# Kernel tuning notes

Hardware: AMD Instinct MI355X
Metric: run time of the kernel (lower is better)

Reference implementation:

```python
import jax, jax.numpy as jnp
import numpy as np

EPS_THRESH = 1e-10   # threshold used by GraphFilter to sparsify A
NORM_EPS = 1e-12     # torch F.normalize clamp
REG = 2.0 / 3.0      # AGE preprocess_graph reg coefficient (layer=1)


def setup_inputs() -> dict:
    key = jax.random.key(0)
    X = jax.random.normal(key, (8192, 512), dtype=jnp.float32)
    return {"X": X}


def reference(X):
    N = X.shape[0]
    # row L2-normalize (torch F.normalize semantics)
    norms = jnp.maximum(jnp.linalg.norm(X, axis=1, keepdims=True), NORM_EPS)
    feats = X / norms
    # dense cosine-similarity graph, thresholded at epsilon
    A = feats @ feats.T                               # [N, N]
    A = jnp.where(A < EPS_THRESH, 0.0, A)
    # remove self-loops (adj - diag_sparse in the original)
    idx = jnp.arange(N)
    A = A.at[idx, idx].set(0.0)
    # preprocess_graph(norm='sym', renorm=True): adj_ = A + I, sym-normalize
    rowsum = jnp.sum(A, axis=1) + 1.0                 # diag of (A + I)
    d_inv_sqrt = rowsum ** -0.5
    A_norm = A * d_inv_sqrt[:, None] * d_inv_sqrt[None, :]
    # A+I normalized: off-diag from A_norm, diag contributes d_i^-1
    diag_term = d_inv_sqrt * d_inv_sqrt               # = 1/rowsum
    # filter = I - reg * (I - (A_norm + diag(diag_term)))
    #        = (1-reg) I + reg * (A_norm + diag(diag_term))
    # propagate: out = filter @ X
    out = (1.0 - REG) * X + REG * (A_norm @ X + (diag_term[:, None] * X))
    return out
```

## Files before the change

kernel.cpp:

```cpp
#include <hip/hip_runtime.h>


#define NR 8192
#define DC 512
#define KZN 4

typedef unsigned short u16;
typedef signed char i8;
typedef float f32x4 __attribute__((ext_vector_type(4)));
typedef int i32x4 __attribute__((ext_vector_type(4)));
typedef u16 u16x4 __attribute__((ext_vector_type(4)));

#define QF_INV 453.5714285f
#define DEQA   4.8608093e-6f
#define QS_INV 254.0f
#define QY_INV 211.6666666f
#define DEQ    1.8600229e-5f

__device__ __forceinline__ float bf2f(u16 u) {
  union { unsigned u; float f; } v; v.u = ((unsigned)u) << 16; return v.f;
}
__device__ __forceinline__ u16 f2bf(float f) {
  union { float f; unsigned u; } v; v.f = f;
  unsigned r = v.u + 0x7fffu + ((v.u >> 16) & 1u);
  return (u16)(r >> 16);
}

__device__ __forceinline__ void async16(const void* ga, void* la) {
  __builtin_amdgcn_global_load_lds(
      (const __attribute__((address_space(1))) unsigned int*)ga,
      (__attribute__((address_space(3))) unsigned int*)la, 16, 0, 0);
}

template <int ROWS, int NT>
__device__ __forceinline__ void stage_i8_k128(const i8* __restrict__ g, int ld,
                                              int row0, int k0, i8* lds, int tid) {
  constexpr int PER = (ROWS * 8) / NT;
#pragma unroll
  for (int q = 0; q < PER; ++q) {
    int s = q * NT + tid;
    int r = s >> 3;
    int kq = (s & 7) ^ (r & 7);
    async16(g + (size_t)(row0 + r) * ld + (k0 + kq * 16), lds + s * 16);
  }
}
__device__ __forceinline__ i32x4 frag_i8_k128(const i8* lds, int m, int c) {
  int phys = c ^ (m & 7);
  return *(const i32x4*)(lds + m * 128 + phys * 16);
}

__global__ __launch_bounds__(256) void k_normalize(const float* __restrict__ X,
                                                   i8* __restrict__ F,
                                                   float* __restrict__ rs_partial) {
  int row = blockIdx.x;
  int tid = threadIdx.x;
  if (tid == 0) rs_partial[row] = 0.f;
  const float* xr = X + (size_t)row * DC;
  float2 v = *(const float2*)(xr + 2 * tid);
  float s = v.x * v.x + v.y * v.y;
#pragma unroll
  for (int off = 32; off; off >>= 1) s += __shfl_down(s, off);
  __shared__ float wsum[4];
  if ((tid & 63) == 0) wsum[tid >> 6] = s;
  __syncthreads();
  float tot = wsum[0] + wsum[1] + wsum[2] + wsum[3];
  float scale = QF_INV / fmaxf(sqrtf(tot), 1e-12f);
  int q0 = (int)rintf(v.x * scale);
  int q1 = (int)rintf(v.y * scale);
  q0 = q0 > 127 ? 127 : (q0 < -127 ? -127 : q0);
  q1 = q1 > 127 ? 127 : (q1 < -127 ? -127 : q1);
  u16 pk = (u16)((q0 & 255) | ((q1 & 255) << 8));
  ((u16*)(F + (size_t)row * DC))[tid] = pk;
}

__global__ __launch_bounds__(256, 4) void k_simgemm(const i8* __restrict__ F,
                                                    i8* __restrict__ S,
                                                    float* __restrict__ rs_partial) {
  __shared__ alignas(16) char smem[32768];
  i8* As = (i8*)smem;
  i8* Bs = (i8*)(smem + 16384);
  int tid = threadIdx.x, lane = tid & 63, wave = tid >> 6;
  int b = blockIdx.x;
  int tj = (int)((sqrtf(8.f * b + 1.f) - 1.f) * 0.5f);
  while ((tj + 1) * (tj + 2) / 2 <= b) ++tj;
  while (tj * (tj + 1) / 2 > b) --tj;
  int ti = b - tj * (tj + 1) / 2;
  bool diag = (ti == tj);

  int wm = wave >> 1, wn = wave & 1;
  int quad = lane >> 4, col = lane & 15;
  i32x4 zero = {0, 0, 0, 0};
  i32x4 acc[4][4];
#pragma unroll
  for (int a = 0; a < 4; ++a)
#pragma unroll
    for (int c = 0; c < 4; ++c) acc[a][c] = zero;

  const i8* Bsrc = diag ? As : Bs;
  for (int kt = 0; kt < DC; kt += 128) {
    __syncthreads();
    stage_i8_k128<128, 256>(F, DC, ti * 128, kt, As, tid);
    if (!diag) stage_i8_k128<128, 256>(F, DC, tj * 128, kt, Bs, tid);
    __syncthreads();
#pragma unroll
    for (int kc = 0; kc < 2; ++kc) {
      i32x4 af[4], bfr[4];
#pragma unroll
      for (int mi = 0; mi < 4; ++mi)
        af[mi] = frag_i8_k128(As, wm * 64 + mi * 16 + col, kc * 4 + quad);
#pragma unroll
      for (int ni = 0; ni < 4; ++ni)
        bfr[ni] = frag_i8_k128(Bsrc, wn * 64 + ni * 16 + col, kc * 4 + quad);
#pragma unroll
      for (int mi = 0; mi < 4; ++mi)
#pragma unroll
        for (int ni = 0; ni < 4; ++ni)
          acc[mi][ni] = __builtin_amdgcn_mfma_i32_16x16x64_i8(af[mi], bfr[ni], acc[mi][ni], 0, 0, 0);
    }
  }

  float av[4][4][4];
  float cs[4] = {0.f, 0.f, 0.f, 0.f};
  float rv[16];
#pragma unroll
  for (int u = 0; u < 16; ++u) rv[u] = 0.f;
#pragma unroll
  for (int mi = 0; mi < 4; ++mi) {
#pragma unroll
    for (int r = 0; r < 4; ++r) {
      int gi = ti * 128 + wm * 64 + mi * 16 + quad * 4 + r;
#pragma unroll
      for (int ni = 0; ni < 4; ++ni) {
        int gj = tj * 128 + wn * 64 + ni * 16 + col;
        float v = (float)acc[mi][ni][r] * DEQA;
        if (v < 1e-10f || gi == gj) v = 0.f;
        av[mi][ni][r] = v;
        cs[ni] += v;
        rv[mi * 4 + r] += v;
      }
    }
  }
#pragma unroll
  for (int ni = 0; ni < 4; ++ni) {
    float c = cs[ni];
    c += __shfl_xor(c, 16);
    c += __shfl_xor(c, 32);
    if (quad == 0) {
      int gj = tj * 128 + wn * 64 + ni * 16 + col;
      atomicAdd(&rs_partial[gj], c);
    }
  }
  if (!diag) {
#pragma unroll
    for (int u = 0; u < 16; ++u) {
      float c = rv[u];
      c += __shfl_xor(c, 1);
      c += __shfl_xor(c, 2);
      c += __shfl_xor(c, 4);
      c += __shfl_xor(c, 8);
      if (col == 0) {
        int mi = u >> 2, r = u & 3;
        int gi = ti * 128 + wm * 64 + mi * 16 + quad * 4 + r;
        atomicAdd(&rs_partial[gi], c);
      }
    }
  }

  char* direct = smem;
  char* mirror = smem + 16384;
  __syncthreads();
#pragma unroll
  for (int mi = 0; mi < 4; ++mi) {
#pragma unroll
    for (int ni = 0; ni < 4; ++ni) {
      int cg = wn * 64 + ni * 16 + col;
      int q[4];
#pragma unroll
      for (int r = 0; r < 4; ++r) {
        int qq = (int)rintf(av[mi][ni][r] * QS_INV);
        q[r] = qq > 127 ? 127 : qq;
      }
#pragma unroll
      for (int r = 0; r < 4; ++r) {
        int row = wm * 64 + mi * 16 + quad * 4 + r;
        int chunk = (cg >> 4) ^ (row & 7);
        direct[row * 128 + chunk * 16 + (cg & 15)] = (char)q[r];
      }
      if (!diag) {
        int mcb = wm * 64 + mi * 16 + quad * 4;
        int chunk = (mcb >> 4) ^ (cg & 7);
        unsigned pk = (unsigned)(q[0] & 255) | ((unsigned)(q[1] & 255) << 8) |
                      ((unsigned)(q[2] & 255) << 16) | ((unsigned)(q[3] & 255) << 24);
        *(unsigned*)(mirror + cg * 128 + chunk * 16 + (mcb & 15)) = pk;
      }
    }
  }
  __syncthreads();
  {
    int r2 = tid >> 1, half = tid & 1;
#pragma unroll
    for (int k = 0; k < 4; ++k) {
      int c = half * 4 + k;
      int phys = c ^ (r2 & 7);
      i32x4 d = *(const i32x4*)(direct + r2 * 128 + phys * 16);
      *(i32x4*)(S + (size_t)(ti * 128 + r2) * NR + tj * 128 + c * 16) = d;
    }
    if (!diag) {
#pragma unroll
      for (int k = 0; k < 4; ++k) {
        int c = half * 4 + k;
        int phys = c ^ (r2 & 7);
        i32x4 d = *(const i32x4*)(mirror + r2 * 128 + phys * 16);
        *(i32x4*)(S + (size_t)(tj * 128 + r2) * NR + ti * 128 + c * 16) = d;
      }
    }
  }
}

__global__ __launch_bounds__(256) void k_make_yt(const float* __restrict__ X,
                                                 const float* __restrict__ rs_partial,
                                                 i8* __restrict__ Yt) {
  __shared__ float T[64][65];
  int i0 = blockIdx.x * 64, k0 = blockIdx.y * 64;
  int tid = threadIdx.x;
  {
    int iL = tid >> 2, ks = (tid & 3) * 4;
    const float* xr = X + (size_t)(i0 + iL) * DC + k0;
#pragma unroll
    for (int u = 0; u < 4; ++u) {
      float4 f = *(const float4*)(xr + ks + u * 16);
      T[iL][ks + u * 16 + 0] = f.x;
      T[iL][ks + u * 16 + 1] = f.y;
      T[iL][ks + u * 16 + 2] = f.z;
      T[iL][ks + u * 16 + 3] = f.w;
    }
  }
  __syncthreads();
  {
    int kL = tid >> 2, ib = (tid & 3) * 16;
    char pk[16];
#pragma unroll
    for (int u = 0; u < 16; ++u) {
      float dj = rsqrtf(rs_partial[i0 + ib + u] + 1.0f);
      float v = T[ib + u][kL] * dj;
      int q = (int)rintf(v * QY_INV);
      q = q > 127 ? 127 : (q < -127 ? -127 : q);
      pk[u] = (char)q;
    }
    *(i32x4*)(Yt + (size_t)(k0 + kL) * NR + i0 + ib) = *(const i32x4*)pk;
  }
}

__global__ __launch_bounds__(512, 4) void k_outgemm(const i8* __restrict__ S,
                                                    const i8* __restrict__ Yt,
                                                    u16* __restrict__ Pb) {
  __shared__ alignas(16) i8 As[128 * 128];
  __shared__ alignas(16) i8 Bs[256 * 128];
  int tid = threadIdx.x, lane = tid & 63, wave = tid >> 6;
  int tn = blockIdx.x, ti = blockIdx.y, kz = blockIdx.z;
  int wm = wave & 1, wn = wave >> 1;
  int quad = lane >> 4, col = lane & 15;
  i32x4 zero = {0, 0, 0, 0};
  i32x4 acc[4][4];
#pragma unroll
  for (int a = 0; a < 4; ++a)
#pragma unroll
    for (int c = 0; c < 4; ++c) acc[a][c] = zero;

  const int KCH = NR / KZN;
  int k_lo = kz * KCH, k_hi = k_lo + KCH;
  for (int kt = k_lo; kt < k_hi; kt += 128) {
    __syncthreads();
    stage_i8_k128<128, 512>(S, NR, ti * 128, kt, As, tid);
    stage_i8_k128<256, 512>(Yt, NR, tn * 256, kt, Bs, tid);
    __syncthreads();
#pragma unroll
    for (int kc = 0; kc < 2; ++kc) {
      i32x4 af[4], bfr[4];
#pragma unroll
      for (int mi = 0; mi < 4; ++mi)
        af[mi] = frag_i8_k128(As, wm * 64 + mi * 16 + col, kc * 4 + quad);
#pragma unroll
      for (int ni = 0; ni < 4; ++ni)
        bfr[ni] = frag_i8_k128(Bs, wn * 64 + ni * 16 + col, kc * 4 + quad);
#pragma unroll
      for (int mi = 0; mi < 4; ++mi)
#pragma unroll
        for (int ni = 0; ni < 4; ++ni)
          acc[mi][ni] = __builtin_amdgcn_mfma_i32_16x16x64_i8(af[mi], bfr[ni], acc[mi][ni], 0, 0, 0);
    }
  }
#pragma unroll
  for (int mi = 0; mi < 4; ++mi) {
#pragma unroll
    for (int r = 0; r < 4; ++r) {
      int gi = ti * 128 + wm * 64 + mi * 16 + quad * 4 + r;
#pragma unroll
      for (int ni = 0; ni < 4; ++ni) {
        int gj = tn * 256 + wn * 64 + ni * 16 + col;
        Pb[((size_t)kz * NR + gi) * DC + gj] = f2bf((float)acc[mi][ni][r] * DEQ);
      }
    }
  }
}

__global__ __launch_bounds__(256) void k_reduce(const u16* __restrict__ Pb,
                                               const float* __restrict__ X,
                                               const float* __restrict__ rs_partial,
                                               float* __restrict__ out) {
  const float c1 = (float)(2.0 / 3.0);
  const float c0 = 1.0f - c1;
  size_t idx = ((size_t)blockIdx.x * 256 + threadIdx.x) * 4;
  int i = (int)(idx >> 9);
  float4 s = {0.f, 0.f, 0.f, 0.f};
#pragma unroll
  for (int kz = 0; kz < KZN; ++kz) {
    u16x4 p = *(const u16x4*)(Pb + (size_t)kz * NR * DC + idx);
    s.x += bf2f(p[0]); s.y += bf2f(p[1]); s.z += bf2f(p[2]); s.w += bf2f(p[3]);
  }
  float4 x = *(const float4*)(X + idx);
  float rs = rs_partial[i] + 1.0f;
  float sc = c1 * rsqrtf(rs);
  float xs = c0 + c1 / rs;
  float4 o = {xs * x.x + sc * s.x, xs * x.y + sc * s.y,
              xs * x.z + sc * s.z, xs * x.w + sc * s.w};
  *(float4*)(out + idx) = o;
}

extern "C" void kernel_launch(void* const* d_in, const int* in_sizes, int n_in,
                              void* d_out, int out_size, void* d_ws, size_t ws_size,
                              hipStream_t stream) {
  const float* X = (const float*)d_in[0];
  float* out = (float*)d_out;
  char* ws = (char*)d_ws;
  i8*  S  = (i8*)(ws);
  i8*  F  = (i8*)(ws + 67108864);
  i8*  Yt = (i8*)(ws + 71303168);
  float* rs_partial = (float*)(ws + 75497472);
  u16* Pb = (u16*)(ws + 75530240);

  k_normalize<<<dim3(NR), dim3(256), 0, stream>>>(X, F, rs_partial);
  k_simgemm<<<dim3(64 * 65 / 2), dim3(256), 0, stream>>>(F, S, rs_partial);
  k_make_yt<<<dim3(128, 8), dim3(256), 0, stream>>>(X, rs_partial, Yt);
  k_outgemm<<<dim3(2, 64, KZN), dim3(512), 0, stream>>>(S, Yt, Pb);
  k_reduce<<<dim3(NR * DC / 1024), dim3(256), 0, stream>>>(Pb, X, rs_partial, out);
}
```

Measured before the change: 182.0 us.

## Load int8 MFMA fragments directly from global with register double-buffering

```diff
diff --git a/kernel.cpp b/kernel.cpp
--- a/kernel.cpp
+++ b/kernel.cpp
@@ -73,12 +73,10 @@
   ((u16*)(F + (size_t)row * DC))[tid] = pk;
 }
 
-__global__ __launch_bounds__(256, 4) void k_simgemm(const i8* __restrict__ F,
+__global__ __launch_bounds__(256, 3) void k_simgemm(const i8* __restrict__ F,
                                                     i8* __restrict__ S,
                                                     float* __restrict__ rs_partial) {
   __shared__ alignas(16) char smem[32768];
-  i8* As = (i8*)smem;
-  i8* Bs = (i8*)(smem + 16384);
   int tid = threadIdx.x, lane = tid & 63, wave = tid >> 6;
   int b = blockIdx.x;
   int tj = (int)((sqrtf(8.f * b + 1.f) - 1.f) * 0.5f);
@@ -96,26 +94,57 @@
 #pragma unroll
     for (int c = 0; c < 4; ++c) acc[a][c] = zero;
 
-  const i8* Bsrc = diag ? As : Bs;
+  const i8* pa = F + ((ti * 128 + wm * 64 + col) * DC + quad * 16);
+  const i8* pb = F + ((tj * 128 + wn * 64 + col) * DC + quad * 16);
+  bool reuse = diag && (wm == wn);
+
+  i32x4 a0[4], b0[4], a1[4], b1[4];
+#pragma unroll
+  for (int mi = 0; mi < 4; ++mi) a0[mi] = *(const i32x4*)(pa + mi * 16 * DC + 0);
+  if (!reuse) {
+#pragma unroll
+    for (int ni = 0; ni < 4; ++ni) b0[ni] = *(const i32x4*)(pb + ni * 16 * DC + 0);
+  }
+#pragma unroll
+  for (int mi = 0; mi < 4; ++mi) a1[mi] = *(const i32x4*)(pa + mi * 16 * DC + 64);
+  if (!reuse) {
+#pragma unroll
+    for (int ni = 0; ni < 4; ++ni) b1[ni] = *(const i32x4*)(pb + ni * 16 * DC + 64);
+  }
+
+#pragma unroll
   for (int kt = 0; kt < DC; kt += 128) {
-    __syncthreads();
-    stage_i8_k128<128, 256>(F, DC, ti * 128, kt, As, tid);
-    if (!diag) stage_i8_k128<128, 256>(F, DC, tj * 128, kt, Bs, tid);
-    __syncthreads();
-#pragma unroll
-    for (int kc = 0; kc < 2; ++kc) {
-      i32x4 af[4], bfr[4];
+    {
+      i32x4* B = reuse ? a0 : b0;
 #pragma unroll
       for (int mi = 0; mi < 4; ++mi)
-        af[mi] = frag_i8_k128(As, wm * 64 + mi * 16 + col, kc * 4 + quad);
-#pragma unroll
-      for (int ni = 0; ni < 4; ++ni)
-        bfr[ni] = frag_i8_k128(Bsrc, wn * 64 + ni * 16 + col, kc * 4 + quad);
+#pragma unroll
+        for (int ni = 0; ni < 4; ++ni)
+          acc[mi][ni] = __builtin_amdgcn_mfma_i32_16x16x64_i8(a0[mi], B[ni], acc[mi][ni], 0, 0, 0);
+      if (kt + 128 < DC) {
+#pragma unroll
+        for (int mi = 0; mi < 4; ++mi) a0[mi] = *(const i32x4*)(pa + mi * 16 * DC + kt + 128);
+        if (!reuse) {
+#pragma unroll
+          for (int ni = 0; ni < 4; ++ni) b0[ni] = *(const i32x4*)(pb + ni * 16 * DC + kt + 128);
+        }
+      }
+    }
+    {
+      i32x4* B = reuse ? a1 : b1;
 #pragma unroll
       for (int mi = 0; mi < 4; ++mi)
 #pragma unroll
         for (int ni = 0; ni < 4; ++ni)
-          acc[mi][ni] = __builtin_amdgcn_mfma_i32_16x16x64_i8(af[mi], bfr[ni], acc[mi][ni], 0, 0, 0);
+          acc[mi][ni] = __builtin_amdgcn_mfma_i32_16x16x64_i8(a1[mi], B[ni], acc[mi][ni], 0, 0, 0);
+      if (kt + 192 < DC) {
+#pragma unroll
+        for (int mi = 0; mi < 4; ++mi) a1[mi] = *(const i32x4*)(pa + mi * 16 * DC + kt + 192);
+        if (!reuse) {
+#pragma unroll
+          for (int ni = 0; ni < 4; ++ni) b1[ni] = *(const i32x4*)(pb + ni * 16 * DC + kt + 192);
+        }
+      }
     }
   }
 
@@ -168,7 +197,6 @@
 
   char* direct = smem;
   char* mirror = smem + 16384;
-  __syncthreads();
 #pragma unroll
   for (int mi = 0; mi < 4; ++mi) {
 #pragma unroll
```

New measurement: 264.3 us. 1.45x slower.
